# Optimization experiments

Hardware: AMD Instinct MI355X
Metric: run time of the kernel (lower is better)

The kernel has to match this reference:

```python
import jax, jax.numpy as jnp
import numpy as np

N = 50000
E = 800000
F_IN = 64
F_OUT = 64


def setup_inputs() -> dict:
    key = jax.random.key(0)
    k1, k2, k3, k4, k5, k6 = jax.random.split(key, 6)
    x = jax.random.normal(k1, (N, F_IN), dtype=jnp.float32)
    x0 = jax.random.normal(k2, (N, F_IN), dtype=jnp.float32)
    edge_index = jax.random.randint(k3, (2, E), 0, N, dtype=jnp.int64)
    # Linear(in_channels, out_channels): weight [out, in], bias [out]
    bound = 1.0 / np.sqrt(F_IN)
    W_w = jax.random.uniform(k4, (F_OUT, F_IN), minval=-bound, maxval=bound, dtype=jnp.float32)
    W_b = jax.random.uniform(k5, (F_OUT,), minval=-bound, maxval=bound, dtype=jnp.float32)
    return {"x": x, "x0": x0, "edge_index": edge_index, "W_w": W_w, "W_b": W_b}


def reference(x, x0, edge_index, W_w, W_b):
    row, col = edge_index[0], edge_index[1]
    n = x.shape[0]
    # degree of each node as a destination (counts of col)
    d = jax.ops.segment_sum(jnp.ones_like(col, dtype=jnp.float32), col, num_segments=n)
    # per-edge symmetric normalization 1/sqrt(d[col]*d[row]); nan_to_num -> 0 where degree 0
    d_in = d[col]
    d_out = d[row]
    value = jnp.where((d_in > 0) & (d_out > 0),
                      jax.lax.rsqrt(jnp.maximum(d_in, 1.0)) * jax.lax.rsqrt(jnp.maximum(d_out, 1.0)),
                      0.0)
    # SpMM: adj has (row=col, col=row) so out[col_e] += value_e * x[row_e]
    msg = value[:, None] * x[row]                     # [E, F]
    agg = jax.ops.segment_sum(msg, col, num_segments=n)  # [N, F]
    # use_init=False, use_weight=True -> dense Linear
    return agg @ W_w.T + W_b
```

## Files before the change

kernel.cpp:

```cpp
#include <hip/hip_runtime.h>

#define NN 50000
#define NE 800000
#define FDIM 64
#define NB 8
#define P1B 768
#define RCAP 256
#define CAP 64
#define OVFCAP 16384
#define NPX 6250
#define GEMMB ((NN + 63) / 64)
#define E4 (NE / 4)
#define CHUNK4 ((E4 + P1B - 1) / P1B)

typedef float f32x4 __attribute__((ext_vector_type(4)));

__device__ __forceinline__ unsigned rne_bf16(float f) {
    unsigned u = __float_as_uint(f);
    return (u + 0x7fffu + ((u >> 16) & 1u)) >> 16;
}

__global__ __launch_bounds__(256) void k_part_gemm(
        const int4* __restrict__ row4, const int4* __restrict__ col4,
        unsigned* __restrict__ buckets, int* __restrict__ bcnt,
        int* __restrict__ cnt, unsigned* __restrict__ ovf, int* __restrict__ ovfcnt,
        const float* __restrict__ x, const float* __restrict__ W,
        unsigned* __restrict__ z) {
    __shared__ float Xl[64][68];
    __shared__ float Wt[64][68];
    int tid = threadIdx.x;

    if (blockIdx.x < P1B) {
        int* lcnt = (int*)&Wt[0][0];
        int gid = blockIdx.x * 256 + tid;
        for (int i = gid; i < NN; i += P1B * 256) cnt[i] = 0;
        if (gid == 0) *ovfcnt = 0;

        if (tid < NB) lcnt[tid] = 0;
        __syncthreads();

        int start = blockIdx.x * CHUNK4;
        int end   = min(start + CHUNK4, E4);
        for (int i = start + tid; i < end; i += 256) {
            int4 r4 = row4[i];
            int4 c4 = col4[i];
            int rr[4] = {r4.x, r4.y, r4.z, r4.w};
            int cc[4] = {c4.x, c4.y, c4.z, c4.w};
#pragma unroll
            for (int t = 0; t < 4; ++t) {
                int c = cc[t];
                int bk = (int)(((unsigned long long)(unsigned)c * 687195ull) >> 32);
                unsigned pk = ((unsigned)rr[t] << 16) | (unsigned)c;
                int slot = atomicAdd(&lcnt[bk], 1);
                if (slot < RCAP)
                    buckets[(size_t)(bk * P1B + blockIdx.x) * RCAP + slot] = pk;
                else {
                    int o = atomicAdd(ovfcnt, 1);
                    if (o >= 0 && o < OVFCAP) ovf[o] = pk;
                }
            }
        }
        __syncthreads();
        if (tid < NB)
            bcnt[tid * P1B + blockIdx.x] = min(lcnt[tid], RCAP);
    } else {
        for (int i = tid; i < FDIM * FDIM; i += 256) {
            int o = i >> 6, k = i & 63;
            Wt[k][o] = W[i];
        }
        int tile = (int)(blockIdx.x - P1B) * 64;
        for (int i = tid; i < 64 * 16; i += 256) {
            int r = i >> 4, c4 = i & 15;
            int gr = tile + r;
            f32x4 v = (gr < NN) ? ((const f32x4*)x)[gr * 16 + c4]
                                : (f32x4){0.f, 0.f, 0.f, 0.f};
            *(f32x4*)&Xl[r][c4 * 4] = v;
        }
        __syncthreads();

        int tr = tid >> 4;
        int tc = tid & 15;

        float acc[4][4] = {};
#pragma unroll 1
        for (int k4 = 0; k4 < 16; ++k4) {
            f32x4 a[4], b[4];
#pragma unroll
            for (int i = 0; i < 4; ++i)
                a[i] = *(const f32x4*)&Xl[tr * 4 + i][k4 * 4];
#pragma unroll
            for (int kk = 0; kk < 4; ++kk)
                b[kk] = *(const f32x4*)&Wt[k4 * 4 + kk][tc * 4];
#pragma unroll
            for (int i = 0; i < 4; ++i) {
#pragma unroll
                for (int jj = 0; jj < 4; ++jj) {
                    acc[i][jj] += a[i].x * b[0][jj] + a[i].y * b[1][jj]
                                + a[i].z * b[2][jj] + a[i].w * b[3][jj];
                }
            }
        }

#pragma unroll
        for (int i = 0; i < 4; ++i) {
            int gr = tile + tr * 4 + i;
            if (gr < NN) {
                unsigned u01 = rne_bf16(acc[i][0]) | (rne_bf16(acc[i][1]) << 16);
                unsigned u23 = rne_bf16(acc[i][2]) | (rne_bf16(acc[i][3]) << 16);
                ((uint2*)z)[gr * 16 + tc] = make_uint2(u01, u23);
            }
        }
    }
}

__global__ __launch_bounds__(256) void k_fill(const unsigned* __restrict__ buckets,
                                              const int* __restrict__ bcnt,
                                              int* __restrict__ cnt,
                                              unsigned short* __restrict__ erow,
                                              unsigned* __restrict__ ovf,
                                              int* __restrict__ ovfcnt) {
    int k  = blockIdx.x & (NB - 1);
    int b1 = blockIdx.x >> 3;
    int m  = bcnt[k * P1B + b1];
    const unsigned* reg = buckets + (size_t)(k * P1B + b1) * RCAP;
    for (int i = threadIdx.x; i < m; i += 256) {
        unsigned pk = reg[i];
        int c = (int)(pk & 0xffffu), r = (int)(pk >> 16);
        int p = atomicAdd(&cnt[c], 1);
        if (p < CAP) erow[c * CAP + p] = (unsigned short)r;
        else {
            int o = atomicAdd(ovfcnt, 1);
            if (o >= 0 && o < OVFCAP) ovf[o] = pk;
        }
    }
}

__global__ __launch_bounds__(256) void k_gather(
        const int* __restrict__ cnt, const unsigned short* __restrict__ erow,
        const uint4* __restrict__ z4, const float* __restrict__ bias,
        const unsigned* __restrict__ ovf, const int* __restrict__ ovfcnt,
        float* __restrict__ out) {
    int lane = threadIdx.x & 63;
    int wv   = threadIdx.x >> 6;
    int xk   = blockIdx.x & 7;
    int sub  = blockIdx.x >> 3;
    int loc  = sub * 4 + wv;
    if (loc >= NPX) return;
    int node = xk * NPX + loc;

    int d  = cnt[node];
    int dc = min(d, CAP);
    int grp = lane >> 3, sl = lane & 7;
    int idx = (lane < dc) ? (int)erow[node * CAP + lane] : 0;

    float a0=0,a1=0,a2=0,a3=0,a4=0,a5=0,a6=0,a7=0;
    int octets = (dc + 7) >> 3;
    for (int j = 0; j < octets; ++j) {
        int ei = j * 8 + grp;
        int rr = __shfl(idx, ei, 64);
        if (ei < dc) {
            int dr = cnt[rr];
            float sr = (dr > 0) ? rsqrtf((float)dr) : 0.f;
            uint4 u = z4[rr * 8 + sl];
            a0 += sr * __uint_as_float(u.x << 16);
            a1 += sr * __uint_as_float(u.x & 0xffff0000u);
            a2 += sr * __uint_as_float(u.y << 16);
            a3 += sr * __uint_as_float(u.y & 0xffff0000u);
            a4 += sr * __uint_as_float(u.z << 16);
            a5 += sr * __uint_as_float(u.z & 0xffff0000u);
            a6 += sr * __uint_as_float(u.w << 16);
            a7 += sr * __uint_as_float(u.w & 0xffff0000u);
        }
    }

    int ovn = min(*ovfcnt, OVFCAP);
    if (ovn > 0) {
        for (int i = 0; i < ovn; ++i) {
            unsigned pk = ovf[i];
            if ((int)(pk & 0xffffu) == node && grp == 0) {
                int rr = (int)(pk >> 16);
                int dr = cnt[rr];
                float sr = (dr > 0) ? rsqrtf((float)dr) : 0.f;
                uint4 u = z4[rr * 8 + sl];
                a0 += sr * __uint_as_float(u.x << 16);
                a1 += sr * __uint_as_float(u.x & 0xffff0000u);
                a2 += sr * __uint_as_float(u.y << 16);
                a3 += sr * __uint_as_float(u.y & 0xffff0000u);
                a4 += sr * __uint_as_float(u.z << 16);
                a5 += sr * __uint_as_float(u.z & 0xffff0000u);
                a6 += sr * __uint_as_float(u.w << 16);
                a7 += sr * __uint_as_float(u.w & 0xffff0000u);
            }
        }
    }

#pragma unroll
    for (int m = 8; m <= 32; m <<= 1) {
        a0 += __shfl_xor(a0, m, 64); a1 += __shfl_xor(a1, m, 64);
        a2 += __shfl_xor(a2, m, 64); a3 += __shfl_xor(a3, m, 64);
        a4 += __shfl_xor(a4, m, 64); a5 += __shfl_xor(a5, m, 64);
        a6 += __shfl_xor(a6, m, 64); a7 += __shfl_xor(a7, m, 64);
    }
    if (grp == 0) {
        float sc = (d > 0) ? rsqrtf((float)d) : 0.f;
        f32x4 b0 = ((const f32x4*)bias)[sl * 2];
        f32x4 b1 = ((const f32x4*)bias)[sl * 2 + 1];
        f32x4 o0 = {sc*a0+b0.x, sc*a1+b0.y, sc*a2+b0.z, sc*a3+b0.w};
        f32x4 o1 = {sc*a4+b1.x, sc*a5+b1.y, sc*a6+b1.z, sc*a7+b1.w};
        __builtin_nontemporal_store(o0, &((f32x4*)out)[node * 16 + sl * 2]);
        __builtin_nontemporal_store(o1, &((f32x4*)out)[node * 16 + sl * 2 + 1]);
    }
}

extern "C" void kernel_launch(void* const* d_in, const int* in_sizes, int n_in,
                              void* d_out, int out_size, void* d_ws, size_t ws_size,
                              hipStream_t stream) {
    const float* x   = (const float*)d_in[0];
    const int*   ei  = (const int*)d_in[2];
    const float* W_w = (const float*)d_in[3];
    const float* W_b = (const float*)d_in[4];
    float*       out = (float*)d_out;

    const int4* row4 = (const int4*)ei;
    const int4* col4 = (const int4*)(ei + NE);

    char* p = (char*)d_ws;
    auto alloc = [&](size_t bytes) {
        char* r = p;
        p += (bytes + 255) & ~(size_t)255;
        return r;
    };
    int*            cnt     = (int*)alloc(NN * sizeof(int));
    int*            ovfcnt  = (int*)alloc(256);
    unsigned*       ovf     = (unsigned*)alloc(OVFCAP * sizeof(unsigned));
    int*            bcnt    = (int*)alloc(NB * P1B * sizeof(int));
    unsigned short* erow    = (unsigned short*)alloc((size_t)NN * CAP * sizeof(unsigned short));
    unsigned*       buckets = (unsigned*)alloc((size_t)NB * P1B * RCAP * sizeof(unsigned));
    unsigned*       z       = (unsigned*)alloc((size_t)NN * FDIM * 2);

    k_part_gemm<<<P1B + GEMMB, 256, 0, stream>>>(row4, col4, buckets, bcnt, cnt,
                                                 ovf, ovfcnt, x, W_w, z);
    k_fill  <<<NB * P1B, 256, 0, stream>>>(buckets, bcnt, cnt, erow, ovf, ovfcnt);
    k_gather<<<NB * ((NPX + 3) / 4), 256, 0, stream>>>(cnt, erow, (const uint4*)z, W_b,
                                                       ovf, ovfcnt, out);
}
```

Baseline: 79.74 us.

## Fuse edge fill and gather into one persistent cooperative kernel with grid sync

Replaces the separate fill and gather launches with a single cooperative kernel of 768 persistent blocks. Each block first inserts edges from 8 bucket regions into the per-node adjacency, then waits on a grid-wide sync, then loops over its share of destination nodes to do the gather, normalization and bias. This removes a kernel boundary and launch gap. In exchange it adds grid-sync overhead and caps resident waves for the latency-bound gather and the atomic-heavy fill.

New measurement: 189.0 us. +137.1%, slower.

```diff
diff --git a/kernel.cpp b/kernel.cpp
--- a/kernel.cpp
+++ b/kernel.cpp
@@ -1,4 +1,7 @@
 #include <hip/hip_runtime.h>
+#include <hip/hip_cooperative_groups.h>
+
+namespace cg = cooperative_groups;
 
 #define NN 50000
 #define NE 800000
@@ -12,6 +15,7 @@
 #define GEMMB ((NN + 63) / 64)
 #define E4 (NE / 4)
 #define CHUNK4 ((E4 + P1B - 1) / P1B)
+#define FGB 768
 
 typedef float f32x4 __attribute__((ext_vector_type(4)));
 
@@ -113,102 +117,106 @@
     }
 }
 
-__global__ __launch_bounds__(256) void k_fill(const unsigned* __restrict__ buckets,
-                                              const int* __restrict__ bcnt,
-                                              int* __restrict__ cnt,
-                                              unsigned short* __restrict__ erow,
-                                              unsigned* __restrict__ ovf,
-                                              int* __restrict__ ovfcnt) {
-    int k  = blockIdx.x & (NB - 1);
-    int b1 = blockIdx.x >> 3;
-    int m  = bcnt[k * P1B + b1];
-    const unsigned* reg = buckets + (size_t)(k * P1B + b1) * RCAP;
-    for (int i = threadIdx.x; i < m; i += 256) {
-        unsigned pk = reg[i];
-        int c = (int)(pk & 0xffffu), r = (int)(pk >> 16);
-        int p = atomicAdd(&cnt[c], 1);
-        if (p < CAP) erow[c * CAP + p] = (unsigned short)r;
-        else {
-            int o = atomicAdd(ovfcnt, 1);
-            if (o >= 0 && o < OVFCAP) ovf[o] = pk;
+__global__ __launch_bounds__(256) void k_fill_gather(
+        const unsigned* __restrict__ buckets, const int* __restrict__ bcnt,
+        int* __restrict__ cnt, unsigned short* __restrict__ erow,
+        const unsigned* __restrict__ z, const float* __restrict__ bias,
+        unsigned* __restrict__ ovf, int* __restrict__ ovfcnt,
+        float* __restrict__ out) {
+    cg::grid_group grid = cg::this_grid();
+    int b   = blockIdx.x;
+    int tid = threadIdx.x;
+    int k   = b & (NB - 1);
+
+#pragma unroll 1
+    for (int j = 0; j < 8; ++j) {
+        int b1 = (b >> 3) + (FGB / NB) * j;
+        int m  = bcnt[k * P1B + b1];
+        if (tid < m) {
+            unsigned pk = buckets[(size_t)(k * P1B + b1) * RCAP + tid];
+            int c = (int)(pk & 0xffffu), r = (int)(pk >> 16);
+            int p = atomicAdd(&cnt[c], 1);
+            if (p < CAP) erow[c * CAP + p] = (unsigned short)r;
+            else {
+                int o = atomicAdd(ovfcnt, 1);
+                if (o >= 0 && o < OVFCAP) ovf[o] = pk;
+            }
         }
     }
-}
-
-__global__ __launch_bounds__(256) void k_gather(
-        const int* __restrict__ cnt, const unsigned short* __restrict__ erow,
-        const uint4* __restrict__ z4, const float* __restrict__ bias,
-        const unsigned* __restrict__ ovf, const int* __restrict__ ovfcnt,
-        float* __restrict__ out) {
-    int lane = threadIdx.x & 63;
-    int wv   = threadIdx.x >> 6;
-    int xk   = blockIdx.x & 7;
-    int sub  = blockIdx.x >> 3;
-    int loc  = sub * 4 + wv;
-    if (loc >= NPX) return;
-    int node = xk * NPX + loc;
-
-    int d  = cnt[node];
-    int dc = min(d, CAP);
-    int grp = lane >> 3, sl = lane & 7;
-    int idx = (lane < dc) ? (int)erow[node * CAP + lane] : 0;
-
-    float a0=0,a1=0,a2=0,a3=0,a4=0,a5=0,a6=0,a7=0;
-    int octets = (dc + 7) >> 3;
-    for (int j = 0; j < octets; ++j) {
-        int ei = j * 8 + grp;
-        int rr = __shfl(idx, ei, 64);
-        if (ei < dc) {
-            int dr = cnt[rr];
-            float sr = (dr > 0) ? rsqrtf((float)dr) : 0.f;
-            uint4 u = z4[rr * 8 + sl];
-            a0 += sr * __uint_as_float(u.x << 16);
-            a1 += sr * __uint_as_float(u.x & 0xffff0000u);
-            a2 += sr * __uint_as_float(u.y << 16);
-            a3 += sr * __uint_as_float(u.y & 0xffff0000u);
-            a4 += sr * __uint_as_float(u.z << 16);
-            a5 += sr * __uint_as_float(u.z & 0xffff0000u);
-            a6 += sr * __uint_as_float(u.w << 16);
-            a7 += sr * __uint_as_float(u.w & 0xffff0000u);
-        }
-    }
-
-    int ovn = min(*ovfcnt, OVFCAP);
-    if (ovn > 0) {
-        for (int i = 0; i < ovn; ++i) {
-            unsigned pk = ovf[i];
-            if ((int)(pk & 0xffffu) == node && grp == 0) {
-                int rr = (int)(pk >> 16);
-                int dr = cnt[rr];
-                float sr = (dr > 0) ? rsqrtf((float)dr) : 0.f;
-                uint4 u = z4[rr * 8 + sl];
-                a0 += sr * __uint_as_float(u.x << 16);
-                a1 += sr * __uint_as_float(u.x & 0xffff0000u);
-                a2 += sr * __uint_as_float(u.y << 16);
-                a3 += sr * __uint_as_float(u.y & 0xffff0000u);
-                a4 += sr * __uint_as_float(u.z << 16);
-                a5 += sr * __uint_as_float(u.z & 0xffff0000u);
-                a6 += sr * __uint_as_float(u.w << 16);
-                a7 += sr * __uint_as_float(u.w & 0xffff0000u);
-            }
-        }
-    }
-
-#pragma unroll
-    for (int m = 8; m <= 32; m <<= 1) {
-        a0 += __shfl_xor(a0, m, 64); a1 += __shfl_xor(a1, m, 64);
-        a2 += __shfl_xor(a2, m, 64); a3 += __shfl_xor(a3, m, 64);
-        a4 += __shfl_xor(a4, m, 64); a5 += __shfl_xor(a5, m, 64);
-        a6 += __shfl_xor(a6, m, 64); a7 += __shfl_xor(a7, m, 64);
-    }
-    if (grp == 0) {
-        float sc = (d > 0) ? rsqrtf((float)d) : 0.f;
-        f32x4 b0 = ((const f32x4*)bias)[sl * 2];
-        f32x4 b1 = ((const f32x4*)bias)[sl * 2 + 1];
-        f32x4 o0 = {sc*a0+b0.x, sc*a1+b0.y, sc*a2+b0.z, sc*a3+b0.w};
-        f32x4 o1 = {sc*a4+b1.x, sc*a5+b1.y, sc*a6+b1.z, sc*a7+b1.w};
-        __builtin_nontemporal_store(o0, &((f32x4*)out)[node * 16 + sl * 2]);
-        __builtin_nontemporal_store(o1, &((f32x4*)out)[node * 16 + sl * 2 + 1]);
+
+    grid.sync();
+
+    {
+        int lane = tid & 63;
+        int wv   = tid >> 6;
+        int grp  = lane >> 3, sl = lane & 7;
+        const uint4* z4 = (const uint4*)z;
+        int ovn = min(*ovfcnt, OVFCAP);
+
+#pragma unroll 1
+        for (int loc = (b >> 3) * 4 + wv; loc < NPX; loc += (FGB / NB) * 4) {
+            int node = k * NPX + loc;
+            int d  = cnt[node];
+            int dc = min(d, CAP);
+            int idx = (lane < dc) ? (int)erow[node * CAP + lane] : 0;
+
+            float a0=0,a1=0,a2=0,a3=0,a4=0,a5=0,a6=0,a7=0;
+            int octets = (dc + 7) >> 3;
+            for (int j = 0; j < octets; ++j) {
+                int ei = j * 8 + grp;
+                int rr = __shfl(idx, ei, 64);
+                if (ei < dc) {
+                    int dr = cnt[rr];
+                    float sr = (dr > 0) ? rsqrtf((float)dr) : 0.f;
+                    uint4 u = z4[rr * 8 + sl];
+                    a0 += sr * __uint_as_float(u.x << 16);
+                    a1 += sr * __uint_as_float(u.x & 0xffff0000u);
+                    a2 += sr * __uint_as_float(u.y << 16);
+                    a3 += sr * __uint_as_float(u.y & 0xffff0000u);
+                    a4 += sr * __uint_as_float(u.z << 16);
+                    a5 += sr * __uint_as_float(u.z & 0xffff0000u);
+                    a6 += sr * __uint_as_float(u.w << 16);
+                    a7 += sr * __uint_as_float(u.w & 0xffff0000u);
+                }
+            }
+
+            if (ovn > 0) {
+                for (int i = 0; i < ovn; ++i) {
+                    unsigned pk = ovf[i];
+                    if ((int)(pk & 0xffffu) == node && grp == 0) {
+                        int rr = (int)(pk >> 16);
+                        int dr = cnt[rr];
+                        float sr = (dr > 0) ? rsqrtf((float)dr) : 0.f;
+                        uint4 u = z4[rr * 8 + sl];
+                        a0 += sr * __uint_as_float(u.x << 16);
+                        a1 += sr * __uint_as_float(u.x & 0xffff0000u);
+                        a2 += sr * __uint_as_float(u.y << 16);
+                        a3 += sr * __uint_as_float(u.y & 0xffff0000u);
+                        a4 += sr * __uint_as_float(u.z << 16);
+                        a5 += sr * __uint_as_float(u.z & 0xffff0000u);
+                        a6 += sr * __uint_as_float(u.w << 16);
+                        a7 += sr * __uint_as_float(u.w & 0xffff0000u);
+                    }
+                }
+            }
+
+#pragma unroll
+            for (int m = 8; m <= 32; m <<= 1) {
+                a0 += __shfl_xor(a0, m, 64); a1 += __shfl_xor(a1, m, 64);
+                a2 += __shfl_xor(a2, m, 64); a3 += __shfl_xor(a3, m, 64);
+                a4 += __shfl_xor(a4, m, 64); a5 += __shfl_xor(a5, m, 64);
+                a6 += __shfl_xor(a6, m, 64); a7 += __shfl_xor(a7, m, 64);
+            }
+            if (grp == 0) {
+                float sc = (d > 0) ? rsqrtf((float)d) : 0.f;
+                f32x4 b0 = ((const f32x4*)bias)[sl * 2];
+                f32x4 b1 = ((const f32x4*)bias)[sl * 2 + 1];
+                f32x4 o0 = {sc*a0+b0.x, sc*a1+b0.y, sc*a2+b0.z, sc*a3+b0.w};
+                f32x4 o1 = {sc*a4+b1.x, sc*a5+b1.y, sc*a6+b1.z, sc*a7+b1.w};
+                __builtin_nontemporal_store(o0, &((f32x4*)out)[node * 16 + sl * 2]);
+                __builtin_nontemporal_store(o1, &((f32x4*)out)[node * 16 + sl * 2 + 1]);
+            }
+        }
     }
 }
 
@@ -240,7 +248,9 @@
 
     k_part_gemm<<<P1B + GEMMB, 256, 0, stream>>>(row4, col4, buckets, bcnt, cnt,
                                                  ovf, ovfcnt, x, W_w, z);
-    k_fill  <<<NB * P1B, 256, 0, stream>>>(buckets, bcnt, cnt, erow, ovf, ovfcnt);
-    k_gather<<<NB * ((NPX + 3) / 4), 256, 0, stream>>>(cnt, erow, (const uint4*)z, W_b,
-                                                       ovf, ovfcnt, out);
-}
+
+    void* args[] = {(void*)&buckets, (void*)&bcnt, (void*)&cnt, (void*)&erow,
+                    (void*)&z, (void*)&W_b, (void*)&ovf, (void*)&ovfcnt, (void*)&out};
+    (void)hipLaunchCooperativeKernel((const void*)k_fill_gather, dim3(FGB), dim3(256),
+                                     args, 0, stream);
+}
```
